# Performance work log

Measured on AMD Instinct MI355X. Metric: run time of the kernel, lower is better.

## Reference

```python
import jax, jax.numpy as jnp
import numpy as np
from jax.scipy.ndimage import map_coordinates

ANGLES = 180
PROJ = 180
IMG = 256
THETA_RAD = np.deg2rad(np.linspace(0.0, 180.0, ANGLES, endpoint=False)).astype(np.float32)


def _ramp_filter(size):
    # skimage _get_fourier_filter(size, 'ramp')
    n = np.concatenate((np.arange(1, size // 2 + 1, 2),
                        np.arange(size // 2 - 1, 0, -2)))
    f = np.zeros(size)
    f[0] = 0.25
    f[1::2] = -1.0 / (np.pi * n) ** 2
    return (2.0 * np.real(np.fft.fft(f))).astype(np.float32)


def radon_t(img, theta):
    # skimage radon(circle=True): rotate by each angle (bilinear warp) and sum rows
    N = img.shape[0]
    center = N // 2
    y, x = jnp.mgrid[0:N, 0:N]
    x = x.astype(jnp.float32)
    y = y.astype(jnp.float32)

    def one(th):
        c, s = jnp.cos(th), jnp.sin(th)
        sx = c * x + s * y - center * (c + s - 1.0)   # source col
        sy = -s * x + c * y - center * (c - s - 1.0)  # source row
        rot = map_coordinates(img, [sy, sx], order=1, mode='constant', cval=0.0)
        return rot.sum(axis=0)  # sum over rows -> [N]

    cols = jax.vmap(one)(theta)  # [A, N]
    return cols.T                # [N, A] sinogram


def iradon_t(sino, theta):
    # skimage iradon(circle=True, filter='ramp', interpolation='linear')
    N, A = sino.shape
    pad = max(64, int(2 ** np.ceil(np.log2(2 * N))))
    filt = jnp.asarray(_ramp_filter(pad))
    proj = jnp.fft.fft(jnp.pad(sino, ((0, pad - N), (0, 0))), axis=0) * filt[:, None]
    filtered = jnp.real(jnp.fft.ifft(proj, axis=0)[:N, :]).astype(jnp.float32)  # [N, A]

    radius = N // 2
    xpr, ypr = jnp.mgrid[0:N, 0:N]
    xpr = (xpr - radius).astype(jnp.float32)
    ypr = (ypr - radius).astype(jnp.float32)

    def one(col, th):
        # detector coordinate t, shifted so index 0 corresponds to x[0] = -N//2
        t = ypr * jnp.cos(th) - xpr * jnp.sin(th) + radius
        i0 = jnp.floor(t).astype(jnp.int32)
        frac = t - i0
        v0 = col[jnp.clip(i0, 0, N - 1)]
        v1 = col[jnp.clip(i0 + 1, 0, N - 1)]
        val = (1.0 - frac) * v0 + frac * v1
        inb = (t >= 0.0) & (t <= N - 1.0)  # np.interp(..., left=0, right=0)
        return jnp.where(inb, val, 0.0)

    back = jax.vmap(one)(filtered.T, theta).sum(axis=0)  # [N, N]
    mask = (xpr ** 2 + ypr ** 2) <= radius ** 2
    return jnp.where(mask, back, 0.0) * (jnp.pi / (2.0 * A))


def setup_inputs() -> dict:
    key = jax.random.key(0)
    ks = jax.random.split(key, 7)
    scale = 1.0 / np.sqrt(PROJ)
    return {
        "x": jax.random.normal(ks[0], (4, 3, IMG, IMG), dtype=jnp.float32),
        "Wq": jax.random.normal(ks[1], (PROJ, PROJ), dtype=jnp.float32) * scale,
        "bq": jax.random.normal(ks[2], (PROJ,), dtype=jnp.float32) * scale,
        "Wk": jax.random.normal(ks[3], (PROJ, PROJ), dtype=jnp.float32) * scale,
        "bk": jax.random.normal(ks[4], (PROJ,), dtype=jnp.float32) * scale,
        "Wv": jax.random.normal(ks[5], (PROJ, PROJ), dtype=jnp.float32) * scale,
        "bv": jax.random.normal(ks[6], (PROJ,), dtype=jnp.float32) * scale,
    }


def reference(x, Wq, bq, Wk, bk, Wv, bv):
    B, C, H, W = x.shape
    theta = jnp.asarray(THETA_RAD)
    imgs = x.reshape(B * C, H, W)
    sino = jax.vmap(lambda im: radon_t(im, theta))(imgs)  # [BC, H, A]
    Q = sino @ Wq.T + bq
    K = sino @ Wk.T + bk
    V = sino @ Wv.T + bv
    scores = jax.nn.softmax(
        jnp.einsum('nij,nkj->nik', Q, K) / jnp.sqrt(jnp.float32(PROJ)), axis=-1)
    att = jnp.einsum('nik,nkj->nij', scores, V)            # [BC, H, A]
    rec = jax.vmap(lambda s: iradon_t(s, theta))(att)      # [BC, H, W]
    return rec.reshape(B, C, H, W)
```

## Files before the change

kernel.cpp:

```cpp
#include <hip/hip_runtime.h>

#define AANG 180
#define NN 256
#define BCH 12

#ifndef M_PI
#define M_PI 3.14159265358979323846
#endif

__device__ __forceinline__ int iclamp(int v, int lo, int hi) {
    return v < lo ? lo : (v > hi ? hi : v);
}

#define LSTR 259
#define LROWSMAX 130

__global__ __launch_bounds__(1024, 1)
void radon_kernel(const float* __restrict__ x, float* __restrict__ partial) {
    __shared__ float tile[LROWSMAX * LSTR];
    __shared__ float red[2][1024];
    int blk = blockIdx.x;
    int g = blk & 31;
    int h = (blk >> 5) & 1;
    int n = blk >> 6;
    int tid = threadIdx.x;
    int lx = tid & 255;
    int qid = tid >> 8;
    int R0 = h ? 127 : -1;
    int nrows = h ? 130 : 129;
    float Ylo = h ? 127.0f : -1.0f;
    float Yhi = h ? 255.0f : 126.0f;
    float Yhi1 = Yhi + 1.0f;
    const float* img = x + (size_t)n * NN * NN;

    for (int rr = qid; rr < nrows; rr += 4) {
        int gr = R0 + rr;
        bool rok = (gr >= 0) && (gr < NN);
        const float* row = img + gr * NN;
        int gc = lx - 1;
        tile[rr * LSTR + lx] = (rok && gc >= 0) ? row[gc] : 0.0f;
        if (lx < 3) {
            int gc2 = 255 + lx;
            tile[rr * LSTR + 256 + lx] = (rok && gc2 < NN) ? row[gc2] : 0.0f;
        }
    }
    __syncthreads();

    float fx = (float)lx;
    int wave = tid >> 6;
    float fxA = (float)((wave & 3) * 64);
    float fxB = fxA + 63.0f;
    int uq0 = qid * 64, uq1 = uq0 + 64;

    for (int aa = 0; aa < 6; ++aa) {
        int a = g + aa * 32;
        if (a >= AANG) break;
        float th = (float)((double)a * (M_PI / 180.0));
        float c = cosf(th), s = sinf(th);
        float kx = -128.0f * (c + s - 1.0f);
        float ky = -128.0f * (c - s - 1.0f);
        float xcon = c * fx + kx;
        float dcon = -s * fx + ky;

        float loY, hiY;
        if (__builtin_fabsf(c) > 1e-5f) {
            float dA = -s * fxA + ky, dB = -s * fxB + ky;
            float t1 = (Ylo - dA) / c, t2 = (Yhi1 - dA) / c;
            float t3 = (Ylo - dB) / c, t4 = (Yhi1 - dB) / c;
            loY = fminf(fminf(t1, t2), fminf(t3, t4));
            hiY = fmaxf(fmaxf(t1, t2), fmaxf(t3, t4));
        } else { loY = 0.0f; hiY = 256.0f; }
        float loX, hiX;
        if (s > 1e-5f) {
            float xA = c * fxA + kx, xB = c * fxB + kx;
            float t1 = (-1.0f - xA) / s, t2 = (257.0f - xA) / s;
            float t3 = (-1.0f - xB) / s, t4 = (257.0f - xB) / s;
            loX = fminf(fminf(t1, t2), fminf(t3, t4));
            hiX = fmaxf(fmaxf(t1, t2), fmaxf(t3, t4));
        } else { loX = 0.0f; hiX = 256.0f; }
        float loF = fmaxf(fmaxf(loY, loX) - 1.0f, 0.0f);
        float hiF = fminf(fminf(hiY, hiX) + 2.0f, 256.0f);
        int us = max(uq0, (int)loF);
        int ue = min(uq1, (int)hiF);
        us = __builtin_amdgcn_readfirstlane(us);
        ue = __builtin_amdgcn_readfirstlane(ue);

        float acc = 0.0f;
        for (int u = us; u < ue; ++u) {
            float fy = (float)u;
            float sy = __builtin_fmaf(c, fy, dcon);
            float sx = __builtin_fmaf(s, fy, xcon);
            float iyf = floorf(sy), ixf = floorf(sx);
            if (iyf >= Ylo && iyf <= Yhi && ixf >= -1.0f && ixf <= 255.0f) {
                float wy = sy - iyf, wx = sx - ixf;
                int lr = (int)iyf - R0;
                int lc = (int)ixf + 1;
                const float* t0 = &tile[lr * LSTR + lc];
                float v00 = t0[0], v01 = t0[1];
                float v10 = t0[LSTR], v11 = t0[LSTR + 1];
                float wx1 = 1.0f - wx, wy1 = 1.0f - wy;
                acc += wy1 * (wx1 * v00 + wx * v01) + wy * (wx1 * v10 + wx * v11);
            }
        }
        int pb = aa & 1;
        red[pb][tid] = acc;
        __syncthreads();
        if (tid < 256) {
            float ssum = red[pb][tid] + red[pb][tid + 256] + red[pb][tid + 512] +
                         red[pb][tid + 768];
            partial[(((size_t)h * BCH + n) * AANG + a) * NN + tid] = ssum;
        }
    }
}

__global__ void wtrans_kernel(const float* __restrict__ Wq, const float* __restrict__ Wk,
                              const float* __restrict__ Wv, float* __restrict__ WqT,
                              float* __restrict__ WkT, float* __restrict__ WvT) {
    int idx = blockIdx.x * 256 + threadIdx.x;
    if (idx < AANG * AANG) {
        int p = idx / AANG;
        int j = idx - p * AANG;
        int src = j * AANG + p;
        WqT[idx] = Wq[src];
        WkT[idx] = Wk[src];
        WvT[idx] = Wv[src];
    }
}

__global__ void qkv_kernel(const float* __restrict__ partial,
                           const float* __restrict__ WqT, const float* __restrict__ bq,
                           const float* __restrict__ WkT, const float* __restrict__ bk,
                           const float* __restrict__ WvT, const float* __restrict__ bv,
                           float* __restrict__ Q, float* __restrict__ Kt,
                           float* __restrict__ V) {
    __shared__ float srow[8][AANG];
    int blk = blockIdx.x;
    int n = blk >> 5;
    int i0 = (blk & 31) * 8;
    int tid = threadIdx.x;
    const size_t HOFF = (size_t)BCH * AANG * NN;
    if (tid < AANG) {
        for (int r = 0; r < 8; ++r) {
            size_t idx = (((size_t)n) * AANG + tid) * NN + (i0 + r);
            srow[r][tid] = partial[idx] + partial[idx + HOFF];
        }
    }
    __syncthreads();
    if (tid < AANG) {
        int j = tid;
        float aq[8], ak[8], av[8];
        float bqv = bq[j], bkv = bk[j], bvv = bv[j];
        for (int r = 0; r < 8; ++r) { aq[r] = bqv; ak[r] = bkv; av[r] = bvv; }
        for (int p = 0; p < AANG; ++p) {
            float wq = WqT[p * AANG + j];
            float wk = WkT[p * AANG + j];
            float wv = WvT[p * AANG + j];
#pragma unroll
            for (int r = 0; r < 8; ++r) {
                float sv = srow[r][p];
                aq[r] += sv * wq;
                ak[r] += sv * wk;
                av[r] += sv * wv;
            }
        }
        for (int r = 0; r < 8; ++r) {
            size_t qb = ((size_t)(n * NN + i0 + r)) * AANG + j;
            Q[qb] = aq[r];
            V[qb] = av[r];
        }
        size_t kb = ((size_t)(n * AANG + j)) * NN + i0;
        for (int r = 0; r < 8; ++r) Kt[kb + r] = ak[r];
    }
}

__global__ void attn_kernel(const float* __restrict__ Q, const float* __restrict__ Kt,
                            const float* __restrict__ V, float* __restrict__ att_t) {
    __shared__ float qrow0[AANG], qrow1[AANG];
    __shared__ float prob0[NN], prob1[NN];
    __shared__ float w0[4], w1[4];
    int blk = blockIdx.x;
    int n = blk >> 7;
    int i0 = (blk & 127) * 2;
    int tid = threadIdx.x;
    int wid = tid >> 6;
    if (tid < AANG) {
        qrow0[tid] = Q[((size_t)(n * NN + i0)) * AANG + tid];
        qrow1[tid] = Q[((size_t)(n * NN + i0 + 1)) * AANG + tid];
    }
    __syncthreads();
    float dot0 = 0.0f, dot1 = 0.0f;
    for (int j = 0; j < AANG; ++j) {
        float kv = Kt[((size_t)(n * AANG + j)) * NN + tid];
        dot0 += qrow0[j] * kv;
        dot1 += qrow1[j] * kv;
    }
    const float rs = 0.0745355992f;
    float l0 = dot0 * rs, l1 = dot1 * rs;
    float m0 = l0, m1 = l1;
    for (int off = 32; off > 0; off >>= 1) {
        m0 = fmaxf(m0, __shfl_xor(m0, off));
        m1 = fmaxf(m1, __shfl_xor(m1, off));
    }
    if ((tid & 63) == 0) { w0[wid] = m0; w1[wid] = m1; }
    __syncthreads();
    float mx0 = fmaxf(fmaxf(w0[0], w0[1]), fmaxf(w0[2], w0[3]));
    float mx1 = fmaxf(fmaxf(w1[0], w1[1]), fmaxf(w1[2], w1[3]));
    float e0 = expf(l0 - mx0), e1 = expf(l1 - mx1);
    float s0 = e0, s1 = e1;
    for (int off = 32; off > 0; off >>= 1) {
        s0 += __shfl_xor(s0, off);
        s1 += __shfl_xor(s1, off);
    }
    __syncthreads();
    if ((tid & 63) == 0) { w0[wid] = s0; w1[wid] = s1; }
    __syncthreads();
    float d0 = w0[0] + w0[1] + w0[2] + w0[3];
    float d1 = w1[0] + w1[1] + w1[2] + w1[3];
    prob0[tid] = e0 / d0;
    prob1[tid] = e1 / d1;
    __syncthreads();
    if (tid < AANG) {
        float acc0 = 0.0f, acc1 = 0.0f;
        const float* vb = V + (size_t)n * NN * AANG + tid;
        for (int k = 0; k < NN; ++k) {
            float v = vb[(size_t)k * AANG];
            acc0 += prob0[k] * v;
            acc1 += prob1[k] * v;
        }
        size_t ob = ((size_t)(n * AANG + tid)) * NN + i0;
        att_t[ob] = acc0;
        att_t[ob + 1] = acc1;
    }
}

__global__ void filter_kernel(const float* __restrict__ att_t, float* __restrict__ filt) {
    __shared__ float col[NN];
    __shared__ float coef[128];
    int blk = blockIdx.x;
    int tid = threadIdx.x;
    col[tid] = att_t[(size_t)blk * NN + tid];
    if (tid < 128) {
        float d = (float)(2 * tid + 1);
        coef[tid] = -2.0f / ((float)(M_PI * M_PI) * d * d);
    }
    __syncthreads();
    float acc = 0.5f * col[tid];
    for (int m = 0; m < 128; ++m) {
        int d = 2 * m + 1;
        float lo = (tid - d >= 0) ? col[tid - d] : 0.0f;
        float hi = (tid + d < NN) ? col[tid + d] : 0.0f;
        acc += coef[m] * (lo + hi);
    }
    filt[(size_t)blk * NN + tid] = acc;
}

#define ACH 12
__global__ void backproj_kernel(const float* __restrict__ filt, float* __restrict__ out) {
    __shared__ float cols[ACH][NN];
    __shared__ float cs[AANG], sn[AANG];
    int blk = blockIdx.x;
    int n = blk >> 8;
    int r = blk & 255;
    int tid = threadIdx.x;
    if (tid < AANG) {
        float th = (float)((double)tid * (M_PI / 180.0));
        cs[tid] = cosf(th);
        sn[tid] = sinf(th);
    }
    float xr = (float)(r - 128);
    float yr = (float)(tid - 128);
    float acc = 0.0f;
    const float* fb = filt + (size_t)n * AANG * NN;
    for (int ch = 0; ch < AANG / ACH; ++ch) {
        __syncthreads();
        for (int q = 0; q < ACH; ++q)
            cols[q][tid] = fb[(size_t)(ch * ACH + q) * NN + tid];
        __syncthreads();
        for (int q = 0; q < ACH; ++q) {
            int aa = ch * ACH + q;
            float t = yr * cs[aa] - xr * sn[aa] + 128.0f;
            float i0f = floorf(t);
            int i0 = (int)i0f;
            float frac = t - i0f;
            int c0 = iclamp(i0, 0, NN - 1);
            int c1 = iclamp(i0 + 1, 0, NN - 1);
            float val = (1.0f - frac) * cols[q][c0] + frac * cols[q][c1];
            if (t >= 0.0f && t <= 255.0f) acc += val;
        }
    }
    bool inside = (xr * xr + yr * yr) <= 16384.0f;
    out[(size_t)blk * NN + tid] = inside ? acc * (float)(M_PI / 360.0) : 0.0f;
}

extern "C" void kernel_launch(void* const* d_in, const int* in_sizes, int n_in,
                              void* d_out, int out_size, void* d_ws, size_t ws_size,
                              hipStream_t stream) {
    const float* x  = (const float*)d_in[0];
    const float* Wq = (const float*)d_in[1];
    const float* bq = (const float*)d_in[2];
    const float* Wk = (const float*)d_in[3];
    const float* bk = (const float*)d_in[4];
    const float* Wv = (const float*)d_in[5];
    const float* bv = (const float*)d_in[6];
    float* out = (float*)d_out;
    float* ws = (float*)d_ws;

    const size_t SZ = (size_t)BCH * NN * AANG;
    float* P     = ws;
    float* Q     = P + 2 * SZ;
    float* Kt    = Q + SZ;
    float* V     = Kt + SZ;
    float* att_t = V + SZ;
    float* WqT   = att_t;
    float* WkT   = WqT + AANG * AANG;
    float* WvT   = WkT + AANG * AANG;
    float* filt  = P;

    wtrans_kernel<<<(AANG * AANG + 255) / 256, 256, 0, stream>>>(Wq, Wk, Wv, WqT, WkT, WvT);
    radon_kernel<<<BCH * 2 * 32, 1024, 0, stream>>>(x, P);
    qkv_kernel<<<BCH * (NN / 8), 256, 0, stream>>>(P, WqT, bq, WkT, bk, WvT, bv, Q, Kt, V);
    attn_kernel<<<BCH * (NN / 2), NN, 0, stream>>>(Q, Kt, V, att_t);
    filter_kernel<<<BCH * AANG, NN, 0, stream>>>(att_t, filt);
    backproj_kernel<<<BCH * NN, NN, 0, stream>>>(filt, out);
}
```

Measured before the change: 486.6 us.

## Pair angles in radon, widen attention rows per block, enlarge backprojection chunks

Radon blocks now process two angles per iteration over 30 angle groups, dropping the per-angle clipping of the row range in favour of full 64-row loops with per-sample bounds tests. Attention processes four query rows per block to reuse K and V loads and stores results as float4. Backprojection loads 36 angle columns per chunk, and unroll pragmas are added to the qkv, filter and backprojection loops. Removing the range pruning adds out-of-bounds iterations in radon, in exchange for more instruction-level parallelism and fewer barriers.

```diff
diff --git a/kernel.cpp b/kernel.cpp
--- a/kernel.cpp
+++ b/kernel.cpp
@@ -20,9 +20,10 @@
     __shared__ float tile[LROWSMAX * LSTR];
     __shared__ float red[2][1024];
     int blk = blockIdx.x;
-    int g = blk & 31;
-    int h = (blk >> 5) & 1;
-    int n = blk >> 6;
+    int g = blk % 30;
+    int t = blk / 30;
+    int h = t & 1;
+    int n = t >> 1;
     int tid = threadIdx.x;
     int lx = tid & 255;
     int qid = tid >> 8;
@@ -30,7 +31,6 @@
     int nrows = h ? 130 : 129;
     float Ylo = h ? 127.0f : -1.0f;
     float Yhi = h ? 255.0f : 126.0f;
-    float Yhi1 = Yhi + 1.0f;
     const float* img = x + (size_t)n * NN * NN;
 
     for (int rr = qid; rr < nrows; rr += 4) {
@@ -47,68 +47,62 @@
     __syncthreads();
 
     float fx = (float)lx;
-    int wave = tid >> 6;
-    float fxA = (float)((wave & 3) * 64);
-    float fxB = fxA + 63.0f;
-    int uq0 = qid * 64, uq1 = uq0 + 64;
-
-    for (int aa = 0; aa < 6; ++aa) {
-        int a = g + aa * 32;
-        if (a >= AANG) break;
-        float th = (float)((double)a * (M_PI / 180.0));
-        float c = cosf(th), s = sinf(th);
-        float kx = -128.0f * (c + s - 1.0f);
-        float ky = -128.0f * (c - s - 1.0f);
-        float xcon = c * fx + kx;
-        float dcon = -s * fx + ky;
-
-        float loY, hiY;
-        if (__builtin_fabsf(c) > 1e-5f) {
-            float dA = -s * fxA + ky, dB = -s * fxB + ky;
-            float t1 = (Ylo - dA) / c, t2 = (Yhi1 - dA) / c;
-            float t3 = (Ylo - dB) / c, t4 = (Yhi1 - dB) / c;
-            loY = fminf(fminf(t1, t2), fminf(t3, t4));
-            hiY = fmaxf(fmaxf(t1, t2), fmaxf(t3, t4));
-        } else { loY = 0.0f; hiY = 256.0f; }
-        float loX, hiX;
-        if (s > 1e-5f) {
-            float xA = c * fxA + kx, xB = c * fxB + kx;
-            float t1 = (-1.0f - xA) / s, t2 = (257.0f - xA) / s;
-            float t3 = (-1.0f - xB) / s, t4 = (257.0f - xB) / s;
-            loX = fminf(fminf(t1, t2), fminf(t3, t4));
-            hiX = fmaxf(fmaxf(t1, t2), fmaxf(t3, t4));
-        } else { loX = 0.0f; hiX = 256.0f; }
-        float loF = fmaxf(fmaxf(loY, loX) - 1.0f, 0.0f);
-        float hiF = fminf(fminf(hiY, hiX) + 2.0f, 256.0f);
-        int us = max(uq0, (int)loF);
-        int ue = min(uq1, (int)hiF);
-        us = __builtin_amdgcn_readfirstlane(us);
-        ue = __builtin_amdgcn_readfirstlane(ue);
-
-        float acc = 0.0f;
-        for (int u = us; u < ue; ++u) {
-            float fy = (float)u;
-            float sy = __builtin_fmaf(c, fy, dcon);
-            float sx = __builtin_fmaf(s, fy, xcon);
-            float iyf = floorf(sy), ixf = floorf(sx);
-            if (iyf >= Ylo && iyf <= Yhi && ixf >= -1.0f && ixf <= 255.0f) {
-                float wy = sy - iyf, wx = sx - ixf;
-                int lr = (int)iyf - R0;
-                int lc = (int)ixf + 1;
+    int ubase = qid * 64;
+
+    for (int pp = 0; pp < 3; ++pp) {
+        int a0 = g + (2 * pp) * 30;
+        int a1 = a0 + 30;
+        float th0 = (float)((double)a0 * (M_PI / 180.0));
+        float th1 = (float)((double)a1 * (M_PI / 180.0));
+        float c0 = cosf(th0), s0 = sinf(th0);
+        float c1 = cosf(th1), s1 = sinf(th1);
+        float kx0 = -128.0f * (c0 + s0 - 1.0f), ky0 = -128.0f * (c0 - s0 - 1.0f);
+        float kx1 = -128.0f * (c1 + s1 - 1.0f), ky1 = -128.0f * (c1 - s1 - 1.0f);
+        float xcon0 = c0 * fx + kx0;
+        float dcon0 = -s0 * fx + ky0;
+        float xcon1 = c1 * fx + kx1;
+        float dcon1 = -s1 * fx + ky1;
+        float acc0 = 0.0f, acc1 = 0.0f;
+#pragma unroll 2
+        for (int i = 0; i < 64; ++i) {
+            float fy = (float)(ubase + i);
+            float sy0 = __builtin_fmaf(c0, fy, dcon0);
+            float sx0 = __builtin_fmaf(s0, fy, xcon0);
+            float sy1 = __builtin_fmaf(c1, fy, dcon1);
+            float sx1 = __builtin_fmaf(s1, fy, xcon1);
+            float iyf0 = floorf(sy0), ixf0 = floorf(sx0);
+            float iyf1 = floorf(sy1), ixf1 = floorf(sx1);
+            if (iyf0 >= Ylo && iyf0 <= Yhi && ixf0 >= -1.0f && ixf0 <= 255.0f) {
+                float wy = sy0 - iyf0, wx = sx0 - ixf0;
+                int lr = (int)iyf0 - R0;
+                int lc = (int)ixf0 + 1;
                 const float* t0 = &tile[lr * LSTR + lc];
                 float v00 = t0[0], v01 = t0[1];
                 float v10 = t0[LSTR], v11 = t0[LSTR + 1];
                 float wx1 = 1.0f - wx, wy1 = 1.0f - wy;
-                acc += wy1 * (wx1 * v00 + wx * v01) + wy * (wx1 * v10 + wx * v11);
+                acc0 += wy1 * (wx1 * v00 + wx * v01) + wy * (wx1 * v10 + wx * v11);
             }
-        }
-        int pb = aa & 1;
-        red[pb][tid] = acc;
+            if (iyf1 >= Ylo && iyf1 <= Yhi && ixf1 >= -1.0f && ixf1 <= 255.0f) {
+                float wy = sy1 - iyf1, wx = sx1 - ixf1;
+                int lr = (int)iyf1 - R0;
+                int lc = (int)ixf1 + 1;
+                const float* t1 = &tile[lr * LSTR + lc];
+                float v00 = t1[0], v01 = t1[1];
+                float v10 = t1[LSTR], v11 = t1[LSTR + 1];
+                float wx1 = 1.0f - wx, wy1 = 1.0f - wy;
+                acc1 += wy1 * (wx1 * v00 + wx * v01) + wy * (wx1 * v10 + wx * v11);
+            }
+        }
+        if (pp) __syncthreads();
+        red[0][tid] = acc0;
+        red[1][tid] = acc1;
         __syncthreads();
         if (tid < 256) {
-            float ssum = red[pb][tid] + red[pb][tid + 256] + red[pb][tid + 512] +
-                         red[pb][tid + 768];
-            partial[(((size_t)h * BCH + n) * AANG + a) * NN + tid] = ssum;
+            float r0 = red[0][tid] + red[0][tid + 256] + red[0][tid + 512] + red[0][tid + 768];
+            float r1 = red[1][tid] + red[1][tid + 256] + red[1][tid + 512] + red[1][tid + 768];
+            size_t base = (((size_t)h * BCH + n) * AANG);
+            partial[(base + a0) * NN + tid] = r0;
+            partial[(base + a1) * NN + tid] = r1;
         }
     }
 }
@@ -151,6 +145,7 @@
         float aq[8], ak[8], av[8];
         float bqv = bq[j], bkv = bk[j], bvv = bv[j];
         for (int r = 0; r < 8; ++r) { aq[r] = bqv; ak[r] = bkv; av[r] = bvv; }
+#pragma unroll 2
         for (int p = 0; p < AANG; ++p) {
             float wq = WqT[p * AANG + j];
             float wk = WkT[p * AANG + j];
@@ -175,61 +170,78 @@
 
 __global__ void attn_kernel(const float* __restrict__ Q, const float* __restrict__ Kt,
                             const float* __restrict__ V, float* __restrict__ att_t) {
-    __shared__ float qrow0[AANG], qrow1[AANG];
-    __shared__ float prob0[NN], prob1[NN];
-    __shared__ float w0[4], w1[4];
-    int blk = blockIdx.x;
-    int n = blk >> 7;
-    int i0 = (blk & 127) * 2;
+    __shared__ float qrow[4][AANG];
+    __shared__ float prob[4][NN];
+    __shared__ float wm[4][4], wsm[4][4];
+    int blk = blockIdx.x;
+    int n = blk >> 6;
+    int i0 = (blk & 63) * 4;
     int tid = threadIdx.x;
     int wid = tid >> 6;
     if (tid < AANG) {
-        qrow0[tid] = Q[((size_t)(n * NN + i0)) * AANG + tid];
-        qrow1[tid] = Q[((size_t)(n * NN + i0 + 1)) * AANG + tid];
-    }
-    __syncthreads();
-    float dot0 = 0.0f, dot1 = 0.0f;
+#pragma unroll
+        for (int r = 0; r < 4; ++r)
+            qrow[r][tid] = Q[((size_t)(n * NN + i0 + r)) * AANG + tid];
+    }
+    __syncthreads();
+    float d0 = 0.0f, d1 = 0.0f, d2 = 0.0f, d3 = 0.0f;
+    const float* kb = Kt + (size_t)n * AANG * NN + tid;
+#pragma unroll 4
     for (int j = 0; j < AANG; ++j) {
-        float kv = Kt[((size_t)(n * AANG + j)) * NN + tid];
-        dot0 += qrow0[j] * kv;
-        dot1 += qrow1[j] * kv;
+        float kv = kb[(size_t)j * NN];
+        d0 += qrow[0][j] * kv;
+        d1 += qrow[1][j] * kv;
+        d2 += qrow[2][j] * kv;
+        d3 += qrow[3][j] * kv;
     }
     const float rs = 0.0745355992f;
-    float l0 = dot0 * rs, l1 = dot1 * rs;
-    float m0 = l0, m1 = l1;
+    float l0 = d0 * rs, l1 = d1 * rs, l2 = d2 * rs, l3 = d3 * rs;
+    float m0 = l0, m1 = l1, m2 = l2, m3 = l3;
     for (int off = 32; off > 0; off >>= 1) {
         m0 = fmaxf(m0, __shfl_xor(m0, off));
         m1 = fmaxf(m1, __shfl_xor(m1, off));
-    }
-    if ((tid & 63) == 0) { w0[wid] = m0; w1[wid] = m1; }
-    __syncthreads();
-    float mx0 = fmaxf(fmaxf(w0[0], w0[1]), fmaxf(w0[2], w0[3]));
-    float mx1 = fmaxf(fmaxf(w1[0], w1[1]), fmaxf(w1[2], w1[3]));
+        m2 = fmaxf(m2, __shfl_xor(m2, off));
+        m3 = fmaxf(m3, __shfl_xor(m3, off));
+    }
+    if ((tid & 63) == 0) { wm[0][wid] = m0; wm[1][wid] = m1; wm[2][wid] = m2; wm[3][wid] = m3; }
+    __syncthreads();
+    float mx0 = fmaxf(fmaxf(wm[0][0], wm[0][1]), fmaxf(wm[0][2], wm[0][3]));
+    float mx1 = fmaxf(fmaxf(wm[1][0], wm[1][1]), fmaxf(wm[1][2], wm[1][3]));
+    float mx2 = fmaxf(fmaxf(wm[2][0], wm[2][1]), fmaxf(wm[2][2], wm[2][3]));
+    float mx3 = fmaxf(fmaxf(wm[3][0], wm[3][1]), fmaxf(wm[3][2], wm[3][3]));
     float e0 = expf(l0 - mx0), e1 = expf(l1 - mx1);
-    float s0 = e0, s1 = e1;
+    float e2 = expf(l2 - mx2), e3 = expf(l3 - mx3);
+    float s0 = e0, s1 = e1, s2 = e2, s3 = e3;
     for (int off = 32; off > 0; off >>= 1) {
         s0 += __shfl_xor(s0, off);
         s1 += __shfl_xor(s1, off);
-    }
-    __syncthreads();
-    if ((tid & 63) == 0) { w0[wid] = s0; w1[wid] = s1; }
-    __syncthreads();
-    float d0 = w0[0] + w0[1] + w0[2] + w0[3];
-    float d1 = w1[0] + w1[1] + w1[2] + w1[3];
-    prob0[tid] = e0 / d0;
-    prob1[tid] = e1 / d1;
-    __syncthreads();
-    if (tid < AANG) {
-        float acc0 = 0.0f, acc1 = 0.0f;
+        s2 += __shfl_xor(s2, off);
+        s3 += __shfl_xor(s3, off);
+    }
+    if ((tid & 63) == 0) { wsm[0][wid] = s0; wsm[1][wid] = s1; wsm[2][wid] = s2; wsm[3][wid] = s3; }
+    __syncthreads();
+    float dn0 = wsm[0][0] + wsm[0][1] + wsm[0][2] + wsm[0][3];
+    float dn1 = wsm[1][0] + wsm[1][1] + wsm[1][2] + wsm[1][3];
+    float dn2 = wsm[2][0] + wsm[2][1] + wsm[2][2] + wsm[2][3];
+    float dn3 = wsm[3][0] + wsm[3][1] + wsm[3][2] + wsm[3][3];
+    prob[0][tid] = e0 / dn0;
+    prob[1][tid] = e1 / dn1;
+    prob[2][tid] = e2 / dn2;
+    prob[3][tid] = e3 / dn3;
+    __syncthreads();
+    if (tid < AANG) {
+        float a0 = 0.0f, a1 = 0.0f, a2 = 0.0f, a3 = 0.0f;
         const float* vb = V + (size_t)n * NN * AANG + tid;
+#pragma unroll 4
         for (int k = 0; k < NN; ++k) {
             float v = vb[(size_t)k * AANG];
-            acc0 += prob0[k] * v;
-            acc1 += prob1[k] * v;
-        }
-        size_t ob = ((size_t)(n * AANG + tid)) * NN + i0;
-        att_t[ob] = acc0;
-        att_t[ob + 1] = acc1;
+            a0 += prob[0][k] * v;
+            a1 += prob[1][k] * v;
+            a2 += prob[2][k] * v;
+            a3 += prob[3][k] * v;
+        }
+        float4 st = make_float4(a0, a1, a2, a3);
+        *(float4*)&att_t[((size_t)(n * AANG + tid)) * NN + i0] = st;
     }
 }
 
@@ -245,6 +257,7 @@
     }
     __syncthreads();
     float acc = 0.5f * col[tid];
+#pragma unroll 4
     for (int m = 0; m < 128; ++m) {
         int d = 2 * m + 1;
         float lo = (tid - d >= 0) ? col[tid - d] : 0.0f;
@@ -254,7 +267,7 @@
     filt[(size_t)blk * NN + tid] = acc;
 }
 
-#define ACH 12
+#define ACH 36
 __global__ void backproj_kernel(const float* __restrict__ filt, float* __restrict__ out) {
     __shared__ float cols[ACH][NN];
     __shared__ float cs[AANG], sn[AANG];
@@ -276,6 +289,7 @@
         for (int q = 0; q < ACH; ++q)
             cols[q][tid] = fb[(size_t)(ch * ACH + q) * NN + tid];
         __syncthreads();
+#pragma unroll 4
         for (int q = 0; q < ACH; ++q) {
             int aa = ch * ACH + q;
             float t = yr * cs[aa] - xr * sn[aa] + 128.0f;
@@ -317,9 +331,9 @@
     float* filt  = P;
 
     wtrans_kernel<<<(AANG * AANG + 255) / 256, 256, 0, stream>>>(Wq, Wk, Wv, WqT, WkT, WvT);
-    radon_kernel<<<BCH * 2 * 32, 1024, 0, stream>>>(x, P);
+    radon_kernel<<<BCH * 2 * 30, 1024, 0, stream>>>(x, P);
     qkv_kernel<<<BCH * (NN / 8), 256, 0, stream>>>(P, WqT, bq, WkT, bk, WvT, bv, Q, Kt, V);
-    attn_kernel<<<BCH * (NN / 2), NN, 0, stream>>>(Q, Kt, V, att_t);
+    attn_kernel<<<BCH * (NN / 4), NN, 0, stream>>>(Q, Kt, V, att_t);
     filter_kernel<<<BCH * AANG, NN, 0, stream>>>(att_t, filt);
     backproj_kernel<<<BCH * NN, NN, 0, stream>>>(filt, out);
 }
```

Result: no change. 491.2 us (+0.9%).
